# Optimization experiments

Measured on AMD Instinct MI355X. Metric: run time of the kernel, lower is better.

## Reference

```python
import jax, jax.numpy as jnp
import numpy as np

L1 = 513          # max_data_length + 1
EMB = 64          # embedding_dim (w)
V = 6             # num_tokens
B = 128           # batch

def setup_inputs() -> dict:
    key = jax.random.key(0)
    k1, k2, k3 = jax.random.split(key, 3)
    src = jax.random.randint(k1, (B, L1), 0, V, dtype=jnp.int64)
    # nn.Embedding default init: N(0,1)
    embedding = jax.random.normal(k2, (V, EMB), dtype=jnp.float32)
    # xavier_uniform over (L1, EMB, L1, V): fan_in = EMB*L1*V? torch treats dim0 as fan_out... use gain scale ~ sqrt(6/(fan_in+fan_out)) with fan computed on flattened dims
    fan_in = EMB * L1 * V
    fan_out = L1
    bound = float(np.sqrt(6.0 / (fan_in + fan_out)))
    weight = jax.random.uniform(k3, (L1, EMB, L1, V), dtype=jnp.float32, minval=-bound, maxval=bound)
    bias = jnp.zeros((L1, V), dtype=jnp.float32)
    return {"src": src, "embedding": embedding, "weight": weight, "bias": bias}

def reference(src, embedding, weight, bias):
    # embedding lookup: (B, L1, EMB)
    x = embedding[src].astype(jnp.float32)
    # causal mask over (s, t): lower-triangular ones
    mask = jnp.tril(jnp.ones((L1, L1), dtype=jnp.float32))
    # batched masked trilinear contraction -> (B, L1, V)
    out = jnp.einsum('bsw,swtv,st->btv', x, weight, mask)
    out = out + bias[None, :, :]
    # permute to (B, V, L1)
    return jnp.transpose(out, (0, 2, 1))
```

## Files before the change

### kernel.cpp

```cpp
#include <hip/hip_runtime.h>
#include <hip/hip_bf16.h>

#define L1C 513
#define EMBC 64
#define VC 6
#define BC 128
#define NCOLS (L1C * VC)
#define NTC 64
#define NTILES ((NCOLS + NTC - 1) / NTC)

#define XELEMS ((size_t)L1C * BC * EMBC)
#define XBYTES (XELEMS * 2)
#define OUTELEMS ((size_t)BC * NCOLS)
#define PARTBYTES (OUTELEMS * 2)

typedef __attribute__((ext_vector_type(8))) short short8;
typedef __attribute__((ext_vector_type(4))) float f32x4;

__device__ __forceinline__ unsigned int pack_bf16x2(float a, float b) {
    __hip_bfloat16 ha = __float2bfloat16(a);
    __hip_bfloat16 hb = __float2bfloat16(b);
    unsigned short ua, ub;
    __builtin_memcpy(&ua, &ha, 2);
    __builtin_memcpy(&ub, &hb, 2);
    return (unsigned int)ua | ((unsigned int)ub << 16);
}

__device__ __forceinline__ unsigned short bf16bits(float a) {
    __hip_bfloat16 h = __float2bfloat16(a);
    unsigned short u;
    __builtin_memcpy(&u, &h, 2);
    return u;
}

__global__ void init_out_kernel(float* __restrict__ out, const float* __restrict__ bias) {
    int i = blockIdx.x * 256 + threadIdx.x;
    if (i >= (int)OUTELEMS) return;
    int r = i % NCOLS;
    int v = r / L1C;
    int t = r - v * L1C;
    out[i] = bias[t * VC + v];
}

__global__ void build_x_kernel(const int* __restrict__ src, const float* __restrict__ emb,
                               unsigned short* __restrict__ X) {
    const int s = blockIdx.x;
    const int b = threadIdx.x >> 1;
    const int half = threadIdx.x & 1;
    const int tok = src[b * L1C + s];
    const float2* e = (const float2*)(emb + tok * EMBC + half * 32);
    unsigned int* row = (unsigned int*)(X + ((size_t)s * BC + b) * EMBC) + half * 16;
#pragma unroll
    for (int i = 0; i < 16; ++i) {
        float2 f = e[i];
        row[i] = pack_bf16x2(f.x, f.y);
    }
}

template <bool PARTIAL>
__global__ __launch_bounds__(256) void gemm_tril_kernel(
    const float* __restrict__ Wt, const unsigned short* __restrict__ X,
    void* __restrict__ outp, int CS) {
    const int tile = blockIdx.x;
    const int chunk = blockIdx.y;
    const int n0 = tile * NTC;
    const int s0 = chunk * CS;
    const int sEnd = min(s0 + CS, L1C);

    __shared__ __align__(16) unsigned short Blds[2][NTC * EMBC];

    const int tid = threadIdx.x;
    const int wid = tid >> 6;
    const int lane = tid & 63;
    const int l15 = lane & 15;
    const int h = lane >> 4;

    const int n = n0 + lane;
    const int tcol = n / VC;
    const size_t nsafe = (n < NCOLS) ? (size_t)n : (size_t)(NCOLS - 1);
    const int wrow0 = wid * 16;
    const int wswz = (lane & 7) << 4;

    f32x4 acc[2][4];
#pragma unroll
    for (int i = 0; i < 2; ++i)
#pragma unroll
        for (int j = 0; j < 4; ++j) acc[i][j] = f32x4{0.f, 0.f, 0.f, 0.f};

    const int sBeg = max(s0, n0 / VC);

#define ISSUEW(ss, farr)                                                         \
    {                                                                            \
        const int scl_ = ((ss) < L1C) ? (ss) : (L1C - 1);                        \
        const float* wb_ = Wt + ((size_t)scl_ * EMBC + wrow0) * NCOLS + nsafe;   \
        _Pragma("unroll") for (int u_ = 0; u_ < 16; ++u_)                        \
            farr[u_] = wb_[(size_t)u_ * NCOLS];                                  \
    }

#define PACKW(ss, farr, buf)                                                     \
    {                                                                            \
        const bool act_ = (tcol <= (ss));                                        \
        char* dr_ = (char*)Blds[buf] + lane * 128;                               \
        _Pragma("unroll") for (int u_ = 0; u_ < 4; ++u_) {                       \
            float g0 = act_ ? farr[u_ * 4 + 0] : 0.f;                            \
            float g1 = act_ ? farr[u_ * 4 + 1] : 0.f;                            \
            float g2 = act_ ? farr[u_ * 4 + 2] : 0.f;                            \
            float g3 = act_ ? farr[u_ * 4 + 3] : 0.f;                            \
            uint2 pk_ = make_uint2(pack_bf16x2(g0, g1), pack_bf16x2(g2, g3));    \
            *(uint2*)(dr_ + ((2 * (wrow0 + u_ * 4)) ^ wswz)) = pk_;              \
        }                                                                        \
    }

#define ISSUEA(ss, aarr)                                                             \
    {                                                                                \
        const int scl_ = ((ss) < L1C) ? (ss) : (L1C - 1);                            \
        const unsigned short* xr_ = X + (size_t)scl_ * (BC * EMBC);                  \
        aarr[0] = *(const short8*)(xr_ + (wid * 32 + l15) * EMBC + h * 8);           \
        aarr[1] = *(const short8*)(xr_ + (wid * 32 + l15) * EMBC + 32 + h * 8);      \
        aarr[2] = *(const short8*)(xr_ + (wid * 32 + 16 + l15) * EMBC + h * 8);      \
        aarr[3] = *(const short8*)(xr_ + (wid * 32 + 16 + l15) * EMBC + 32 + h * 8); \
    }

#define MFMASTEP(aarr, buf)                                                                              \
    {                                                                                                    \
        _Pragma("unroll") for (int kk_ = 0; kk_ < 2; ++kk_) {                                            \
            const int foff_ = (kk_ * 64 + h * 16) ^ ((l15 & 7) << 4);                                    \
            _Pragma("unroll") for (int nt_ = 0; nt_ < 4; ++nt_) {                                        \
                short8 bb_ = *(const short8*)((const char*)Blds[buf] + (nt_ * 16 + l15) * 128 + foff_);  \
                acc[0][nt_] = __builtin_amdgcn_mfma_f32_16x16x32_bf16(aarr[kk_], bb_, acc[0][nt_], 0, 0, 0);     \
                acc[1][nt_] = __builtin_amdgcn_mfma_f32_16x16x32_bf16(aarr[2 + kk_], bb_, acc[1][nt_], 0, 0, 0); \
            }                                                                                            \
        }                                                                                                \
    }

    if (sBeg < sEnd) {
        float fW0[16], fW1[16];
        short8 aC[4], aN[4];
        {
            float fP[16];
            ISSUEW(sBeg, fP);
            PACKW(sBeg, fP, 0);
        }
        ISSUEW(sBeg + 1, fW0);
        ISSUEA(sBeg, aC);
        __syncthreads();

        int s = sBeg, cur = 0;
        while (true) {
            ISSUEW(s + 2, fW1);
            ISSUEA(s + 1, aN);
            MFMASTEP(aC, cur);
            PACKW(s + 1, fW0, cur ^ 1);
            __syncthreads();
            cur ^= 1;
            ++s;
            if (s >= sEnd) break;

            ISSUEW(s + 2, fW0);
            ISSUEA(s + 1, aC);
            MFMASTEP(aN, cur);
            PACKW(s + 1, fW1, cur ^ 1);
            __syncthreads();
            cur ^= 1;
            ++s;
            if (s >= sEnd) break;
        }
    }

#pragma unroll
    for (int nt = 0; nt < 4; ++nt) {
        const int nn = n0 + nt * 16 + l15;
        if (nn >= NCOLS) continue;
        if (PARTIAL) {
            unsigned short* dst = (unsigned short*)outp + (size_t)chunk * OUTELEMS;
#pragma unroll
            for (int ms = 0; ms < 2; ++ms)
#pragma unroll
                for (int r = 0; r < 4; ++r) {
                    const int bi = wid * 32 + ms * 16 + h * 4 + r;
                    dst[(size_t)bi * NCOLS + nn] = bf16bits(acc[ms][nt][r]);
                }
        } else {
            float* dst = (float*)outp;
            const int t = nn / VC;
            const int v = nn - t * VC;
            const size_t obase = (size_t)v * L1C + t;
#pragma unroll
            for (int ms = 0; ms < 2; ++ms)
#pragma unroll
                for (int r = 0; r < 4; ++r) {
                    const int bi = wid * 32 + ms * 16 + h * 4 + r;
                    atomicAdd(dst + (size_t)bi * NCOLS + obase, acc[ms][nt][r]);
                }
        }
    }
#undef ISSUEW
#undef PACKW
#undef ISSUEA
#undef MFMASTEP
}

__global__ void reduce_kernel(const unsigned short* __restrict__ partial,
                              const float* __restrict__ bias,
                              float* __restrict__ out, int nchunks) {
    int i4 = blockIdx.x * 256 + threadIdx.x;
    if (i4 >= (int)(OUTELEMS / 4)) return;
    const size_t base = (size_t)i4 * 4;
    float sum[4];
#pragma unroll
    for (int j = 0; j < 4; ++j) {
        int idx = (int)base + j;
        sum[j] = bias[idx % NCOLS];
    }
    for (int c = 0; c < nchunks; ++c) {
        const ushort4 p = *(const ushort4*)(partial + (size_t)c * OUTELEMS + base);
        unsigned int u0 = (unsigned int)p.x << 16, u1 = (unsigned int)p.y << 16;
        unsigned int u2 = (unsigned int)p.z << 16, u3 = (unsigned int)p.w << 16;
        float f0, f1, f2, f3;
        __builtin_memcpy(&f0, &u0, 4);
        __builtin_memcpy(&f1, &u1, 4);
        __builtin_memcpy(&f2, &u2, 4);
        __builtin_memcpy(&f3, &u3, 4);
        sum[0] += f0;
        sum[1] += f1;
        sum[2] += f2;
        sum[3] += f3;
    }
#pragma unroll
    for (int j = 0; j < 4; ++j) {
        int idx = (int)base + j;
        int b = idx / NCOLS;
        int nn = idx - b * NCOLS;
        int t = nn / VC;
        int v = nn - t * VC;
        out[(size_t)b * NCOLS + (size_t)v * L1C + t] = sum[j];
    }
}

extern "C" void kernel_launch(void* const* d_in, const int* in_sizes, int n_in,
                              void* d_out, int out_size, void* d_ws, size_t ws_size,
                              hipStream_t stream) {
    const int* src = (const int*)d_in[0];
    const float* emb = (const float*)d_in[1];
    const float* wt = (const float*)d_in[2];
    const float* bias = (const float*)d_in[3];
    float* out = (float*)d_out;
    unsigned short* X = (unsigned short*)d_ws;

    build_x_kernel<<<L1C, 256, 0, stream>>>(src, emb, X);

    size_t avail = (ws_size > XBYTES) ? (ws_size - XBYTES) : 0;
    int nchunks = (int)(avail / PARTBYTES);
    if (nchunks > 31) nchunks = 31;

    if (nchunks >= 2) {
        int CS = (L1C + nchunks - 1) / nchunks;
        nchunks = (L1C + CS - 1) / CS;
        unsigned short* partial = (unsigned short*)((char*)d_ws + XBYTES);
        dim3 grid(NTILES, nchunks);
        gemm_tril_kernel<true><<<grid, 256, 0, stream>>>(wt, X, (void*)partial, CS);
        reduce_kernel<<<(int)((OUTELEMS / 4 + 255) / 256), 256, 0, stream>>>(partial, bias, out, nchunks);
    } else {
        init_out_kernel<<<(int)((OUTELEMS + 255) / 256), 256, 0, stream>>>(out, bias);
        dim3 grid(NTILES, 17);
        gemm_tril_kernel<false><<<grid, 256, 0, stream>>>(wt, X, (void*)out, 31);
    }
}
```

Measured before the change: 93.12 us.

## Use fine fixed chunks, XCD-aware tile remap, early exit, and skip empty partials in reduce

```diff
diff --git a/kernel.cpp b/kernel.cpp
--- a/kernel.cpp
+++ b/kernel.cpp
@@ -8,6 +8,8 @@
 #define NCOLS (L1C * VC)
 #define NTC 64
 #define NTILES ((NCOLS + NTC - 1) / NTC)
+#define CSC 8
+#define NCHUNK ((L1C + CSC - 1) / CSC)
 
 #define XELEMS ((size_t)L1C * BC * EMBC)
 #define XBYTES (XELEMS * 2)
@@ -58,14 +60,20 @@
 }
 
 template <bool PARTIAL>
-__global__ __launch_bounds__(256) void gemm_tril_kernel(
+__global__ __launch_bounds__(256, 4) void gemm_tril_kernel(
     const float* __restrict__ Wt, const unsigned short* __restrict__ X,
     void* __restrict__ outp, int CS) {
-    const int tile = blockIdx.x;
+    const int xb = blockIdx.x;
+    const int xcd = xb & 7;
+    const int pos = xb >> 3;
+    const int tile = ((xcd == 0) ? 0 : (7 + (xcd - 1) * 6)) + pos;
+
     const int chunk = blockIdx.y;
     const int n0 = tile * NTC;
     const int s0 = chunk * CS;
     const int sEnd = min(s0 + CS, L1C);
+    const int sBeg = max(s0, n0 / VC);
+    if (sBeg >= sEnd) return;
 
     __shared__ __align__(16) unsigned short Blds[2][NTC * EMBC];
 
@@ -86,8 +94,6 @@
     for (int i = 0; i < 2; ++i)
 #pragma unroll
         for (int j = 0; j < 4; ++j) acc[i][j] = f32x4{0.f, 0.f, 0.f, 0.f};
-
-    const int sBeg = max(s0, n0 / VC);
 
 #define ISSUEW(ss, farr)                                                         \
     {                                                                            \
@@ -113,8 +119,7 @@
 
 #define ISSUEA(ss, aarr)                                                             \
     {                                                                                \
-        const int scl_ = ((ss) < L1C) ? (ss) : (L1C - 1);                            \
-        const unsigned short* xr_ = X + (size_t)scl_ * (BC * EMBC);                  \
+        const unsigned short* xr_ = X + (size_t)(ss) * (BC * EMBC);                  \
         aarr[0] = *(const short8*)(xr_ + (wid * 32 + l15) * EMBC + h * 8);           \
         aarr[1] = *(const short8*)(xr_ + (wid * 32 + l15) * EMBC + 32 + h * 8);      \
         aarr[2] = *(const short8*)(xr_ + (wid * 32 + 16 + l15) * EMBC + h * 8);      \
@@ -133,37 +138,31 @@
         }                                                                                                \
     }
 
-    if (sBeg < sEnd) {
+    {
         float fW0[16], fW1[16];
-        short8 aC[4], aN[4];
-        {
-            float fP[16];
-            ISSUEW(sBeg, fP);
-            PACKW(sBeg, fP, 0);
-        }
+        short8 aC[4];
+        ISSUEW(sBeg, fW1);
+        PACKW(sBeg, fW1, 0);
         ISSUEW(sBeg + 1, fW0);
-        ISSUEA(sBeg, aC);
         __syncthreads();
 
         int s = sBeg, cur = 0;
         while (true) {
+            ISSUEA(s, aC);
             ISSUEW(s + 2, fW1);
-            ISSUEA(s + 1, aN);
             MFMASTEP(aC, cur);
             PACKW(s + 1, fW0, cur ^ 1);
             __syncthreads();
             cur ^= 1;
-            ++s;
-            if (s >= sEnd) break;
-
+            if (++s >= sEnd) break;
+
+            ISSUEA(s, aC);
             ISSUEW(s + 2, fW0);
-            ISSUEA(s + 1, aC);
-            MFMASTEP(aN, cur);
+            MFMASTEP(aC, cur);
             PACKW(s + 1, fW1, cur ^ 1);
             __syncthreads();
             cur ^= 1;
-            ++s;
-            if (s >= sEnd) break;
+            if (++s >= sEnd) break;
         }
     }
 
@@ -202,17 +201,24 @@
 
 __global__ void reduce_kernel(const unsigned short* __restrict__ partial,
                               const float* __restrict__ bias,
-                              float* __restrict__ out, int nchunks) {
+                              float* __restrict__ out, int nchunks, int CS) {
     int i4 = blockIdx.x * 256 + threadIdx.x;
     if (i4 >= (int)(OUTELEMS / 4)) return;
     const size_t base = (size_t)i4 * 4;
     float sum[4];
+    int cf[4];
+    int cmin = 1 << 30;
 #pragma unroll
     for (int j = 0; j < 4; ++j) {
         int idx = (int)base + j;
-        sum[j] = bias[idx % NCOLS];
-    }
-    for (int c = 0; c < nchunks; ++c) {
+        int nn = idx % NCOLS;
+        sum[j] = bias[nn];
+        int tl = nn >> 6;
+        int tmin = (tl << 6) / VC;
+        cf[j] = tmin / CS;
+        cmin = min(cmin, cf[j]);
+    }
+    for (int c = cmin; c < nchunks; ++c) {
         const ushort4 p = *(const ushort4*)(partial + (size_t)c * OUTELEMS + base);
         unsigned int u0 = (unsigned int)p.x << 16, u1 = (unsigned int)p.y << 16;
         unsigned int u2 = (unsigned int)p.z << 16, u3 = (unsigned int)p.w << 16;
@@ -221,10 +227,10 @@
         __builtin_memcpy(&f1, &u1, 4);
         __builtin_memcpy(&f2, &u2, 4);
         __builtin_memcpy(&f3, &u3, 4);
-        sum[0] += f0;
-        sum[1] += f1;
-        sum[2] += f2;
-        sum[3] += f3;
+        if (c >= cf[0]) sum[0] += f0;
+        if (c >= cf[1]) sum[1] += f1;
+        if (c >= cf[2]) sum[2] += f2;
+        if (c >= cf[3]) sum[3] += f3;
     }
 #pragma unroll
     for (int j = 0; j < 4; ++j) {
@@ -249,17 +255,20 @@
 
     build_x_kernel<<<L1C, 256, 0, stream>>>(src, emb, X);
 
-    size_t avail = (ws_size > XBYTES) ? (ws_size - XBYTES) : 0;
-    int nchunks = (int)(avail / PARTBYTES);
-    if (nchunks > 31) nchunks = 31;
-
-    if (nchunks >= 2) {
+    if (ws_size >= XBYTES + (size_t)NCHUNK * PARTBYTES) {
+        unsigned short* partial = (unsigned short*)((char*)d_ws + XBYTES);
+        dim3 grid(NTILES, NCHUNK);
+        gemm_tril_kernel<true><<<grid, 256, 0, stream>>>(wt, X, (void*)partial, CSC);
+        reduce_kernel<<<(int)((OUTELEMS / 4 + 255) / 256), 256, 0, stream>>>(partial, bias, out, NCHUNK, CSC);
+    } else if (ws_size >= XBYTES + 2 * PARTBYTES) {
+        int nchunks = (int)((ws_size - XBYTES) / PARTBYTES);
+        if (nchunks > NCHUNK) nchunks = NCHUNK;
         int CS = (L1C + nchunks - 1) / nchunks;
         nchunks = (L1C + CS - 1) / CS;
         unsigned short* partial = (unsigned short*)((char*)d_ws + XBYTES);
         dim3 grid(NTILES, nchunks);
         gemm_tril_kernel<true><<<grid, 256, 0, stream>>>(wt, X, (void*)partial, CS);
-        reduce_kernel<<<(int)((OUTELEMS / 4 + 255) / 256), 256, 0, stream>>>(partial, bias, out, nchunks);
+        reduce_kernel<<<(int)((OUTELEMS / 4 + 255) / 256), 256, 0, stream>>>(partial, bias, out, nchunks, CS);
     } else {
         init_out_kernel<<<(int)((OUTELEMS + 255) / 256), 256, 0, stream>>>(out, bias);
         dim3 grid(NTILES, 17);
```

Result: slower. 103.4 us (+11.1%).
